# Performance work log

Measured on AMD Instinct MI355X. Metric: run time of the kernel, lower is better.

## Reference

```python
import jax, jax.numpy as jnp
import numpy as np

N = 50000          # nodes
E = 800000         # edges (before self-loops)
IN = 128           # in_channels
C = 32             # hidden_channels
H = 4              # heads
SLOPE = 0.2        # PyG GATConv default negative_slope
NUM_CLASSES = 2


def setup_inputs() -> dict:
    key = jax.random.key(0)
    ks = jax.random.split(key, 20)
    s = 0.1
    inp = {
        "x": jax.random.normal(ks[0], (N, IN), jnp.float32),
        "edge_index": jax.random.randint(ks[1], (2, E), 0, N, jnp.int64),
        # conv1: IN -> H*C (concat)
        "W1": jax.random.normal(ks[2], (IN, H * C), jnp.float32) * s,
        "a1_src": jax.random.normal(ks[3], (H, C), jnp.float32) * s,
        "a1_dst": jax.random.normal(ks[4], (H, C), jnp.float32) * s,
        "b1": jnp.zeros((H * C,), jnp.float32),
        # conv2: H*C -> H*C (concat)
        "W2": jax.random.normal(ks[5], (H * C, H * C), jnp.float32) * s,
        "a2_src": jax.random.normal(ks[6], (H, C), jnp.float32) * s,
        "a2_dst": jax.random.normal(ks[7], (H, C), jnp.float32) * s,
        "b2": jnp.zeros((H * C,), jnp.float32),
        # conv3: H*C -> C (heads=1, concat=False)
        "W3": jax.random.normal(ks[8], (H * C, C), jnp.float32) * s,
        "a3_src": jax.random.normal(ks[9], (1, C), jnp.float32) * s,
        "a3_dst": jax.random.normal(ks[10], (1, C), jnp.float32) * s,
        "b3": jnp.zeros((C,), jnp.float32),
        # node classification head: C -> 2
        "Wc": jax.random.normal(ks[11], (C, NUM_CLASSES), jnp.float32) * s,
        "bc": jnp.zeros((NUM_CLASSES,), jnp.float32),
    }
    return inp


def gat_conv(x, src, dst, W, a_src, a_dst, b, heads, out_c, concat):
    """PyG-style GATConv with self-loops already appended to (src, dst)."""
    n = x.shape[0]
    h = (x @ W).reshape(n, heads, out_c)            # [N,H,C]
    al_src = jnp.sum(h * a_src, axis=-1)            # [N,H]
    al_dst = jnp.sum(h * a_dst, axis=-1)            # [N,H]
    e = al_src[src] + al_dst[dst]                   # [Et,H]
    e = jax.nn.leaky_relu(e, SLOPE)
    # numerically-stable segment softmax over edges sharing a destination
    emax = jax.ops.segment_max(e, dst, num_segments=n)   # every node has a self-loop
    e = jnp.exp(e - emax[dst])
    denom = jax.ops.segment_sum(e, dst, num_segments=n)
    alpha = e / (denom[dst] + 1e-16)                # [Et,H]
    msg = h[src] * alpha[:, :, None]                # [Et,H,C]
    out = jax.ops.segment_sum(msg, dst, num_segments=n)  # [N,H,C]
    out = out.reshape(n, heads * out_c) if concat else jnp.mean(out, axis=1)
    return out + b


def reference(x, edge_index, W1, a1_src, a1_dst, b1, W2, a2_src, a2_dst, b2,
              W3, a3_src, a3_dst, b3, Wc, bc):
    n = x.shape[0]
    loop = jnp.arange(n, dtype=edge_index.dtype)
    src = jnp.concatenate([edge_index[0], loop])
    dst = jnp.concatenate([edge_index[1], loop])
    h = jax.nn.elu(gat_conv(x, src, dst, W1, a1_src, a1_dst, b1, H, C, True))
    h = jax.nn.elu(gat_conv(h, src, dst, W2, a2_src, a2_dst, b2, H, C, True))
    h = gat_conv(h, src, dst, W3, a3_src, a3_dst, b3, 1, C, False)
    node_output = h @ Wc + bc                       # [N,2]
    link_embedding = h                              # [N,C]
    return (node_output, link_embedding)
```

## Files before the change

### kernel.cpp

```cpp
#include <hip/hip_runtime.h>
#include <math.h>

#define SLOPE 0.2f

__device__ __forceinline__ float lrelu(float x) { return x > 0.f ? x : SLOPE * x; }

__device__ __forceinline__ float bflo(unsigned int u) { return __uint_as_float(u << 16); }
__device__ __forceinline__ float bfhi(unsigned int u) { return __uint_as_float(u & 0xffff0000u); }
__device__ __forceinline__ unsigned short f2bf(float f) {
    unsigned int u = __float_as_uint(f);
    unsigned int r = u + 0x7fffu + ((u >> 16) & 1u);
    return (unsigned short)(r >> 16);
}

typedef short frag8 __attribute__((ext_vector_type(8)));
typedef float f32x4 __attribute__((ext_vector_type(4)));

__global__ __launch_bounds__(256) void wtrans_kernel(
    const float* __restrict__ W1, const float* __restrict__ W2,
    unsigned short* __restrict__ Wt1, unsigned short* __restrict__ Wt2,
    int* __restrict__ bcnt, int nbcnt)
{
    int idx = blockIdx.x * 256 + threadIdx.x;
    if (idx < nbcnt) bcnt[idx] = 0;
    const float* W = W1;
    unsigned short* Wt = Wt1;
    int i = idx;
    if (idx >= 16384) { W = W2; Wt = Wt2; i = idx - 16384; }
    int n = i >> 7, k = i & 127;
    Wt[i] = f2bf(W[k * 128 + n]);
}

#define TF_MB 64
#define TF_LDK 136

template <bool BF16IN>
__device__ __forceinline__ void transform_body(
    int bid, const void* __restrict__ xin, const unsigned short* __restrict__ Wt,
    const float* __restrict__ a_src, const float* __restrict__ a_dst,
    unsigned short* __restrict__ hout, float* __restrict__ alsrc,
    float* __restrict__ aldst, int N,
    unsigned short* xs, unsigned short* wt)
{
    constexpr int MB = TF_MB;
    constexpr int LDK = TF_LDK;

    const int node0 = bid * MB;
    const int t = threadIdx.x;

    if constexpr (BF16IN) {
        const unsigned short* xb = (const unsigned short*)xin;
        for (int i = t; i < MB * 16; i += 256) {
            int row = i >> 4, c16 = i & 15;
            uint4 v = make_uint4(0u, 0u, 0u, 0u);
            if (node0 + row < N)
                v = ((const uint4*)(xb + (size_t)(node0 + row) * 128))[c16];
            *(uint4*)&xs[row * LDK + c16 * 8] = v;
        }
    } else {
        const float* xf = (const float*)xin;
        for (int i = t; i < MB * 32; i += 256) {
            int row = i >> 5, col4 = i & 31;
            ushort4 o;
            if (node0 + row < N) {
                float4 v = ((const float4*)(xf + (size_t)(node0 + row) * 128))[col4];
                o.x = f2bf(v.x); o.y = f2bf(v.y); o.z = f2bf(v.z); o.w = f2bf(v.w);
            } else {
                o.x = o.y = o.z = o.w = 0;
            }
            *(ushort4*)&xs[row * LDK + col4 * 4] = o;
        }
    }
    for (int i = t; i < 2048; i += 256) {
        int n = i >> 4, k16 = i & 15;
        uint4 v = ((const uint4*)Wt)[i];
        *(uint4*)&wt[n * LDK + k16 * 8] = v;
    }
    __syncthreads();

    const int w    = t >> 6;
    const int lane = t & 63;
    const int r    = lane & 15;
    const int q    = lane >> 4;

    f32x4 acc[4][2];
#pragma unroll
    for (int mt = 0; mt < 4; ++mt)
#pragma unroll
        for (int nl = 0; nl < 2; ++nl)
            acc[mt][nl] = (f32x4){0.f, 0.f, 0.f, 0.f};

#pragma unroll
    for (int kk = 0; kk < 4; ++kk) {
        const int kof = kk * 32 + q * 8;
        frag8 b0 = *(const frag8*)&wt[(w * 32 + r) * LDK + kof];
        frag8 b1 = *(const frag8*)&wt[(w * 32 + 16 + r) * LDK + kof];
#pragma unroll
        for (int mt = 0; mt < 4; ++mt) {
            frag8 a = *(const frag8*)&xs[(mt * 16 + r) * LDK + kof];
            acc[mt][0] = __builtin_amdgcn_mfma_f32_16x16x32_bf16(a, b0, acc[mt][0], 0, 0, 0);
            acc[mt][1] = __builtin_amdgcn_mfma_f32_16x16x32_bf16(a, b1, acc[mt][1], 0, 0, 0);
        }
    }

    const float as0 = a_src[w * 32 + r],      ad0 = a_dst[w * 32 + r];
    const float as1 = a_src[w * 32 + 16 + r], ad1 = a_dst[w * 32 + 16 + r];
#pragma unroll
    for (int mt = 0; mt < 4; ++mt) {
#pragma unroll
        for (int reg = 0; reg < 4; ++reg) {
            float s = acc[mt][0][reg] * as0 + acc[mt][1][reg] * as1;
            float d = acc[mt][0][reg] * ad0 + acc[mt][1][reg] * ad1;
#pragma unroll
            for (int off = 1; off < 16; off <<= 1) {
                s += __shfl_xor(s, off);
                d += __shfl_xor(d, off);
            }
            if (r == 0) {
                int m = mt * 16 + q * 4 + reg;
                int n = node0 + m;
                if (n < N) {
                    alsrc[n * 4 + w] = s;
                    aldst[n * 4 + w] = d;
                }
            }
        }
    }

    __syncthreads();
#pragma unroll
    for (int mt = 0; mt < 4; ++mt)
#pragma unroll
        for (int nl = 0; nl < 2; ++nl)
#pragma unroll
            for (int reg = 0; reg < 4; ++reg) {
                int m = mt * 16 + q * 4 + reg;
                int n = w * 32 + nl * 16 + r;
                xs[m * LDK + n] = f2bf(acc[mt][nl][reg]);
            }
    __syncthreads();
    {
        int row = t >> 2, cbase = (t & 3) * 32;
        if (node0 + row < N) {
            uint4* dst = (uint4*)(hout + (size_t)(node0 + row) * 128 + cbase);
#pragma unroll
            for (int j = 0; j < 4; ++j)
                dst[j] = *(const uint4*)&xs[row * LDK + cbase + j * 8];
        }
    }
}

template <bool BF16IN>
__global__ __launch_bounds__(256) void transform_mfma_kernel(
    const void* __restrict__ xin, const unsigned short* __restrict__ Wt,
    const float* __restrict__ a_src, const float* __restrict__ a_dst,
    unsigned short* __restrict__ hout, float* __restrict__ alsrc,
    float* __restrict__ aldst, int N)
{
    __shared__ __align__(16) unsigned short xs[TF_MB * TF_LDK];
    __shared__ __align__(16) unsigned short wt[128 * TF_LDK];
    transform_body<BF16IN>(blockIdx.x, xin, Wt, a_src, a_dst, hout,
                           alsrc, aldst, N, xs, wt);
}

template <int COUT, int Hh, int NPT>
__global__ __launch_bounds__(256) void transform_kernel(
    const unsigned short* __restrict__ xin, const float* __restrict__ W,
    const float* __restrict__ a_src, const float* __restrict__ a_dst,
    unsigned short* __restrict__ hout, float* __restrict__ alsrc,
    float* __restrict__ aldst, int N)
{
    constexpr int JT = COUT / 4;
    constexpr int GROUPS = 256 / JT;
    constexpr int NB = GROUPS * NPT;
    constexpr int PAD = 4;
    __shared__ __align__(16) float xs[NB][128 + PAD];

    const int node0 = blockIdx.x * NB;
    for (int i = threadIdx.x; i < NB * 16; i += 256) {
        int row = i >> 4, c16 = i & 15;
        uint4 v = make_uint4(0u, 0u, 0u, 0u);
        if (node0 + row < N)
            v = ((const uint4*)(xin + (size_t)(node0 + row) * 128))[c16];
        float* xp = &xs[row][c16 * 8];
        xp[0] = bflo(v.x); xp[1] = bfhi(v.x);
        xp[2] = bflo(v.y); xp[3] = bfhi(v.y);
        xp[4] = bflo(v.z); xp[5] = bfhi(v.z);
        xp[6] = bflo(v.w); xp[7] = bfhi(v.w);
    }
    __syncthreads();

    const int jt = threadIdx.x % JT;
    const int g  = threadIdx.x / JT;
    const int j4 = jt * 4;

    float4 acc[NPT];
#pragma unroll
    for (int m = 0; m < NPT; ++m) acc[m] = make_float4(0.f, 0.f, 0.f, 0.f);

    const float4* Wf4 = (const float4*)W;
    for (int k4 = 0; k4 < 32; ++k4) {
        float4 w0 = Wf4[(4 * k4 + 0) * JT + jt];
        float4 w1 = Wf4[(4 * k4 + 1) * JT + jt];
        float4 w2 = Wf4[(4 * k4 + 2) * JT + jt];
        float4 w3 = Wf4[(4 * k4 + 3) * JT + jt];
#pragma unroll
        for (int m = 0; m < NPT; ++m) {
            float4 xv = *(const float4*)&xs[g * NPT + m][k4 << 2];
            acc[m].x += xv.x * w0.x + xv.y * w1.x + xv.z * w2.x + xv.w * w3.x;
            acc[m].y += xv.x * w0.y + xv.y * w1.y + xv.z * w2.y + xv.w * w3.y;
            acc[m].z += xv.x * w0.z + xv.y * w1.z + xv.z * w2.z + xv.w * w3.z;
            acc[m].w += xv.x * w0.w + xv.y * w1.w + xv.z * w2.w + xv.w * w3.w;
        }
    }

    const float4 as4 = ((const float4*)a_src)[jt];
    const float4 ad4 = ((const float4*)a_dst)[jt];
    const int hh = j4 >> 5;

#pragma unroll
    for (int m = 0; m < NPT; ++m) {
        int n = node0 + g * NPT + m;
        float4 v = acc[m];
        float sv = v.x * as4.x + v.y * as4.y + v.z * as4.z + v.w * as4.w;
        float dv = v.x * ad4.x + v.y * ad4.y + v.z * ad4.z + v.w * ad4.w;
#pragma unroll
        for (int off = 4; off >= 1; off >>= 1) {
            sv += __shfl_xor(sv, off);
            dv += __shfl_xor(dv, off);
        }
        if (n < N) {
            ushort4 hp;
            hp.x = f2bf(v.x); hp.y = f2bf(v.y);
            hp.z = f2bf(v.z); hp.w = f2bf(v.w);
            ((ushort4*)(hout + (size_t)n * COUT))[jt] = hp;
            if ((jt & 7) == 0) {
                alsrc[n * Hh + hh] = sv;
                aldst[n * Hh + hh] = dv;
            }
        }
    }
}

#define BKT_CAP 2048
#define NBKT_MAX 1024
#define CH_BIN 4096

__device__ __forceinline__ void bin_body(
    int bid, const int* __restrict__ src, const int* __restrict__ dst,
    int* __restrict__ bcnt, unsigned int* __restrict__ tmp, int E, int nbkt,
    int* hist, int* base)
{
    const int e0 = bid * CH_BIN;
    const int e1 = min(e0 + CH_BIN, E);

    for (int b = threadIdx.x; b < nbkt; b += 256) hist[b] = 0;
    __syncthreads();
    for (int e = e0 + threadIdx.x; e < e1; e += 256) {
        int d = __builtin_nontemporal_load(dst + e);
        atomicAdd(&hist[d >> 6], 1);
    }
    __syncthreads();
    for (int b = threadIdx.x; b < nbkt; b += 256) {
        int c = hist[b];
        base[b] = (c > 0) ? atomicAdd(&bcnt[b << 4], c) : 0;
        hist[b] = 0;
    }
    __syncthreads();
    for (int e = e0 + threadIdx.x; e < e1; e += 256) {
        int d = __builtin_nontemporal_load(dst + e);
        int s = __builtin_nontemporal_load(src + e);
        int b = d >> 6;
        int pos = base[b] + atomicAdd(&hist[b], 1);
        if (pos < BKT_CAP)
            tmp[((size_t)b << 11) + pos] =
                ((unsigned int)s << 6) | (unsigned int)(d & 63);
    }
}

template <bool BF16IN>
__global__ __launch_bounds__(256) void bin_transform_kernel(
    const int* __restrict__ src, const int* __restrict__ dst,
    int* __restrict__ bcnt, unsigned int* __restrict__ tmp, int E, int nbkt,
    const void* __restrict__ xin, const unsigned short* __restrict__ Wt,
    const float* __restrict__ a_src, const float* __restrict__ a_dst,
    unsigned short* __restrict__ hout, float* __restrict__ alsrc,
    float* __restrict__ aldst, int N, int nbin)
{
    __shared__ __align__(16) unsigned short smem[TF_MB * TF_LDK + 128 * TF_LDK];
    if ((int)blockIdx.x < nbin) {
        int* hist = (int*)smem;
        bin_body(blockIdx.x, src, dst, bcnt, tmp, E, nbkt, hist, hist + NBKT_MAX);
    } else {
        transform_body<BF16IN>(blockIdx.x - nbin, xin, Wt, a_src, a_dst,
                               hout, alsrc, aldst, N, smem, smem + TF_MB * TF_LDK);
    }
}

__global__ __launch_bounds__(256) void bucket_csr_kernel(
    const unsigned int* __restrict__ tmp, const int* __restrict__ bcnt,
    int* __restrict__ deg, int* __restrict__ offsets,
    int* __restrict__ src_sorted, int N)
{
    int b = blockIdx.x;
    __shared__ int hist[64];
    if (threadIdx.x < 64) hist[threadIdx.x] = 0;
    __syncthreads();
    int cnt = min(bcnt[b << 4], BKT_CAP);
    const unsigned int* tb = tmp + ((size_t)b << 11);
    for (int i = threadIdx.x; i < cnt; i += 256)
        atomicAdd(&hist[tb[i] & 63u], 1);
    __syncthreads();
    if (threadIdx.x < 64) {
        int v = hist[threadIdx.x];
        int incl = v;
#pragma unroll
        for (int off = 1; off < 64; off <<= 1) {
            int t2 = __shfl_up(incl, off);
            if ((int)threadIdx.x >= off) incl += t2;
        }
        int excl = incl - v;
        int node = (b << 6) + threadIdx.x;
        if (node < N) {
            deg[node] = v;
            offsets[node] = (b << 11) + excl;
        }
        hist[threadIdx.x] = excl;
    }
    __syncthreads();
    for (int i = threadIdx.x; i < cnt; i += 256) {
        unsigned int p = tb[i];
        int pos = atomicAdd(&hist[p & 63u], 1);
        src_sorted[((size_t)b << 11) + pos] = (int)(p >> 6);
    }
}

__device__ __forceinline__ void fma8(const uint4& p, float w, float* a) {
    a[0] += w * bflo(p.x); a[1] += w * bfhi(p.x);
    a[2] += w * bflo(p.y); a[3] += w * bfhi(p.y);
    a[4] += w * bflo(p.z); a[5] += w * bfhi(p.z);
    a[6] += w * bflo(p.w); a[7] += w * bfhi(p.w);
}

template <int Hh, int Cc, bool DO_ELU, bool OUTBF, bool FUSE_HEAD>
__global__ __launch_bounds__(256) void gat_agg_kernel(
    const int* __restrict__ offsets, const int* __restrict__ deg_arr,
    const int* __restrict__ src_sorted,
    const unsigned short* __restrict__ h, const float* __restrict__ alsrc,
    const float* __restrict__ aldst, const float* __restrict__ bias,
    void* __restrict__ outv, const float* __restrict__ Wc,
    const float* __restrict__ bc, float* __restrict__ node_out, int N)
{
    constexpr int HC  = Hh * Cc;
    constexpr int TPN = HC / 8;
    constexpr int NPB = 256 / TPN;
    constexpr int CHUNK = 32;
    constexpr int CH_STRIDE = CHUNK + 4;
    constexpr int PLANE = NPB * CH_STRIDE + 8;
    __shared__ int   s_src[NPB][CHUNK];
    __shared__ __align__(16) float s_w[Hh * PLANE];
    __shared__ int   s_nch[NPB];

    const int g  = threadIdx.x / TPN;
    const int lt = threadIdx.x % TPN;
    const int n  = blockIdx.x * NPB + g;
    const bool valid = n < N;

    int off0 = 0, deg = 0;
    if (valid) { off0 = offsets[n]; deg = deg_arr[n]; }
    if (lt == 0) s_nch[g] = (deg + CHUNK - 1) / CHUNK;
    __syncthreads();
    int maxch = 0;
#pragma unroll
    for (int i = 0; i < NPB; ++i) maxch = max(maxch, s_nch[i]);

    const int hh = (lt * 8) / Cc;
    float adv[Hh];
    if (valid) {
        if constexpr (Hh == 4) {
            float4 t = ((const float4*)aldst)[n];
            adv[0] = t.x; adv[1] = t.y; adv[2] = t.z; adv[3] = t.w;
        } else {
            adv[0] = aldst[n];
        }
    }

    const uint4* h4 = (const uint4*)h;

    uint4 pself = make_uint4(0u, 0u, 0u, 0u);
    float als_self = 0.f;
    if (valid) {
        pself = h4[(size_t)n * TPN + lt];
        als_self = alsrc[n * Hh + hh];
    }

    const int wbase = hh * PLANE + g * CH_STRIDE;

    float a[8] = {0.f, 0.f, 0.f, 0.f, 0.f, 0.f, 0.f, 0.f};
    float den = 0.f;
    for (int ch = 0; ch < maxch; ++ch) {
        int base = ch * CHUNK;
        int cnt = deg - base;
        cnt = cnt < 0 ? 0 : (cnt > CHUNK ? CHUNK : cnt);
        __syncthreads();
        for (int i = lt; i < cnt; i += TPN) {
            int s = __builtin_nontemporal_load(src_sorted + off0 + base + i);
            s_src[g][i] = s;
            if constexpr (Hh == 4) {
                float4 av = ((const float4*)alsrc)[s];
                s_w[0 * PLANE + g * CH_STRIDE + i] = __expf(lrelu(av.x + adv[0]));
                s_w[1 * PLANE + g * CH_STRIDE + i] = __expf(lrelu(av.y + adv[1]));
                s_w[2 * PLANE + g * CH_STRIDE + i] = __expf(lrelu(av.z + adv[2]));
                s_w[3 * PLANE + g * CH_STRIDE + i] = __expf(lrelu(av.w + adv[3]));
            } else {
                s_w[g * CH_STRIDE + i] = __expf(lrelu(alsrc[s] + adv[0]));
            }
        }
        __syncthreads();
        int i = 0;
        for (; i + 3 < cnt; i += 4) {
            int s0 = s_src[g][i],     s1 = s_src[g][i + 1];
            int s2 = s_src[g][i + 2], s3 = s_src[g][i + 3];
            float4 wv = *(const float4*)&s_w[wbase + i];
            uint4 p0 = h4[(size_t)s0 * TPN + lt];
            uint4 p1 = h4[(size_t)s1 * TPN + lt];
            uint4 p2 = h4[(size_t)s2 * TPN + lt];
            uint4 p3 = h4[(size_t)s3 * TPN + lt];
            fma8(p0, wv.x, a);
            fma8(p1, wv.y, a);
            fma8(p2, wv.z, a);
            fma8(p3, wv.w, a);
            den += (wv.x + wv.y) + (wv.z + wv.w);
        }
        for (; i < cnt; ++i) {
            int s0 = s_src[g][i];
            float w0 = s_w[wbase + i];
            uint4 p0 = h4[(size_t)s0 * TPN + lt];
            fma8(p0, w0, a);
            den += w0;
        }
    }

    if (valid) {
        float wself = __expf(lrelu(als_self + adv[hh]));
        fma8(pself, wself, a);
        den += wself + 1e-16f;
        float inv = 1.f / den;
        float4 bv0 = ((const float4*)bias)[lt * 2];
        float4 bv1 = ((const float4*)bias)[lt * 2 + 1];
        float o[8];
        o[0] = a[0] * inv + bv0.x; o[1] = a[1] * inv + bv0.y;
        o[2] = a[2] * inv + bv0.z; o[3] = a[3] * inv + bv0.w;
        o[4] = a[4] * inv + bv1.x; o[5] = a[5] * inv + bv1.y;
        o[6] = a[6] * inv + bv1.z; o[7] = a[7] * inv + bv1.w;
        if (DO_ELU) {
#pragma unroll
            for (int q = 0; q < 8; ++q)
                o[q] = o[q] > 0.f ? o[q] : __expf(o[q]) - 1.f;
        }
        if constexpr (OUTBF) {
            unsigned short* ob = (unsigned short*)outv;
            uint4 pk;
            pk.x = (unsigned int)f2bf(o[0]) | ((unsigned int)f2bf(o[1]) << 16);
            pk.y = (unsigned int)f2bf(o[2]) | ((unsigned int)f2bf(o[3]) << 16);
            pk.z = (unsigned int)f2bf(o[4]) | ((unsigned int)f2bf(o[5]) << 16);
            pk.w = (unsigned int)f2bf(o[6]) | ((unsigned int)f2bf(o[7]) << 16);
            ((uint4*)(ob + (size_t)n * HC))[lt] = pk;
        } else {
            float* of = (float*)outv;
            float4* op = (float4*)(of + (size_t)n * HC);
            op[lt * 2]     = make_float4(o[0], o[1], o[2], o[3]);
            op[lt * 2 + 1] = make_float4(o[4], o[5], o[6], o[7]);
        }
        if constexpr (FUSE_HEAD) {
            float s0 = 0.f, s1 = 0.f;
#pragma unroll
            for (int q = 0; q < 8; ++q) {
                int c = lt * 8 + q;
                s0 += o[q] * Wc[c * 2];
                s1 += o[q] * Wc[c * 2 + 1];
            }
            s0 += __shfl_xor(s0, 1); s0 += __shfl_xor(s0, 2);
            s1 += __shfl_xor(s1, 1); s1 += __shfl_xor(s1, 2);
            if (lt == 0) {
                node_out[(size_t)n * 2]     = s0 + bc[0];
                node_out[(size_t)n * 2 + 1] = s1 + bc[1];
            }
        }
    }
}

extern "C" void kernel_launch(void* const* d_in, const int* in_sizes, int n_in,
                              void* d_out, int out_size, void* d_ws, size_t ws_size,
                              hipStream_t stream)
{
    const float* x   = (const float*)d_in[0];
    const int*   ei  = (const int*)d_in[1];
    const float* W1  = (const float*)d_in[2];
    const float* a1s = (const float*)d_in[3];
    const float* a1d = (const float*)d_in[4];
    const float* b1  = (const float*)d_in[5];
    const float* W2  = (const float*)d_in[6];
    const float* a2s = (const float*)d_in[7];
    const float* a2d = (const float*)d_in[8];
    const float* b2  = (const float*)d_in[9];
    const float* W3  = (const float*)d_in[10];
    const float* a3s = (const float*)d_in[11];
    const float* a3d = (const float*)d_in[12];
    const float* b3  = (const float*)d_in[13];
    const float* Wc  = (const float*)d_in[14];
    const float* bc  = (const float*)d_in[15];

    const int N = in_sizes[0] / 128;
    const int E = in_sizes[1] / 2;
    const int* srcIdx = ei;
    const int* dstIdx = ei + E;

    const int NBKT = (N + 63) >> 6;

    float* alsrc = (float*)d_ws;
    float* aldst = alsrc + (size_t)N * 4;
    unsigned short* fb16 = (unsigned short*)(aldst + (size_t)N * 4);
    unsigned short* hbuf = fb16 + (size_t)N * 128;
    int* deg        = (int*)(hbuf + (size_t)N * 128);
    int* offsets    = deg + N;
    uintptr_t wp = ((uintptr_t)(offsets + N) + 15) & ~(uintptr_t)15;
    unsigned short* wt1 = (unsigned short*)wp;
    unsigned short* wt2 = wt1 + 16384;
    int* bcnt       = (int*)(wt2 + 16384);
    int* src_sorted = bcnt + (size_t)NBKT * 16;
    unsigned int* tmp = (unsigned int*)(src_sorted + (size_t)NBKT * BKT_CAP);

    float* node_out = (float*)d_out;
    float* link_out = node_out + (size_t)N * 2;

    const int nbBin = (E + CH_BIN - 1) / CH_BIN;
    const int nbT   = (N + 63) / 64;

    wtrans_kernel<<<128, 256, 0, stream>>>(W1, W2, wt1, wt2, bcnt, NBKT * 16);

    bin_transform_kernel<false><<<nbBin + nbT, 256, 0, stream>>>(
        srcIdx, dstIdx, bcnt, tmp, E, NBKT,
        x, wt1, a1s, a1d, hbuf, alsrc, aldst, N, nbBin);

    bucket_csr_kernel<<<NBKT, 256, 0, stream>>>(tmp, bcnt, deg, offsets,
                                                src_sorted, N);

    gat_agg_kernel<4, 32, true, true, false><<<(N + 15) / 16, 256, 0, stream>>>(
        offsets, deg, src_sorted, hbuf, alsrc, aldst, b1, fb16,
        nullptr, nullptr, nullptr, N);

    transform_mfma_kernel<true><<<nbT, 256, 0, stream>>>(
        fb16, wt2, a2s, a2d, hbuf, alsrc, aldst, N);
    gat_agg_kernel<4, 32, true, true, false><<<(N + 15) / 16, 256, 0, stream>>>(
        offsets, deg, src_sorted, hbuf, alsrc, aldst, b2, fb16,
        nullptr, nullptr, nullptr, N);

    transform_kernel<32, 1, 4><<<(N + 127) / 128, 256, 0, stream>>>(
        fb16, W3, a3s, a3d, hbuf, alsrc, aldst, N);
    gat_agg_kernel<1, 32, false, false, true><<<(N + 63) / 64, 256, 0, stream>>>(
        offsets, deg, src_sorted, hbuf, alsrc, aldst, b3, link_out,
        Wc, bc, node_out, N);
}
```

Before: 271.3 us.

## Fuse layer aggregation with next-layer linear transform into single kernels

Merges each layer's GAT aggregation with the following layer's weight transform. The aggregated features stay in shared memory (bf16 for the MFMA layer-2 path, fp32 for the VALU layer-3 path) and never round-trip through global memory. Each layer gets its own h/alpha buffers, so the fused kernels never read and write the same buffer. This removes two launches and the intermediate feature writes and reads. In exchange, each block now handles 64 nodes in four sequential 16-node passes with more __syncthreads, and it holds the large shared-memory footprint during the aggregation phase, which may lower occupancy and hide less of the gather latency.

```diff
diff --git a/kernel.cpp b/kernel.cpp
--- a/kernel.cpp
+++ b/kernel.cpp
@@ -34,50 +34,14 @@
 #define TF_MB 64
 #define TF_LDK 136
 
-template <bool BF16IN>
-__device__ __forceinline__ void transform_body(
-    int bid, const void* __restrict__ xin, const unsigned short* __restrict__ Wt,
-    const float* __restrict__ a_src, const float* __restrict__ a_dst,
+__device__ __forceinline__ void transform_compute(
+    int node0, const float* __restrict__ a_src, const float* __restrict__ a_dst,
     unsigned short* __restrict__ hout, float* __restrict__ alsrc,
     float* __restrict__ aldst, int N,
-    unsigned short* xs, unsigned short* wt)
-{
-    constexpr int MB = TF_MB;
+    unsigned short* xs, const unsigned short* wt)
+{
     constexpr int LDK = TF_LDK;
-
-    const int node0 = bid * MB;
     const int t = threadIdx.x;
-
-    if constexpr (BF16IN) {
-        const unsigned short* xb = (const unsigned short*)xin;
-        for (int i = t; i < MB * 16; i += 256) {
-            int row = i >> 4, c16 = i & 15;
-            uint4 v = make_uint4(0u, 0u, 0u, 0u);
-            if (node0 + row < N)
-                v = ((const uint4*)(xb + (size_t)(node0 + row) * 128))[c16];
-            *(uint4*)&xs[row * LDK + c16 * 8] = v;
-        }
-    } else {
-        const float* xf = (const float*)xin;
-        for (int i = t; i < MB * 32; i += 256) {
-            int row = i >> 5, col4 = i & 31;
-            ushort4 o;
-            if (node0 + row < N) {
-                float4 v = ((const float4*)(xf + (size_t)(node0 + row) * 128))[col4];
-                o.x = f2bf(v.x); o.y = f2bf(v.y); o.z = f2bf(v.z); o.w = f2bf(v.w);
-            } else {
-                o.x = o.y = o.z = o.w = 0;
-            }
-            *(ushort4*)&xs[row * LDK + col4 * 4] = o;
-        }
-    }
-    for (int i = t; i < 2048; i += 256) {
-        int n = i >> 4, k16 = i & 15;
-        uint4 v = ((const uint4*)Wt)[i];
-        *(uint4*)&wt[n * LDK + k16 * 8] = v;
-    }
-    __syncthreads();
-
     const int w    = t >> 6;
     const int lane = t & 63;
     const int r    = lane & 15;
@@ -150,96 +114,35 @@
     }
 }
 
-template <bool BF16IN>
-__global__ __launch_bounds__(256) void transform_mfma_kernel(
-    const void* __restrict__ xin, const unsigned short* __restrict__ Wt,
+__device__ __forceinline__ void transform_body_f32(
+    int bid, const float* __restrict__ xf, const unsigned short* __restrict__ Wt,
     const float* __restrict__ a_src, const float* __restrict__ a_dst,
     unsigned short* __restrict__ hout, float* __restrict__ alsrc,
-    float* __restrict__ aldst, int N)
-{
-    __shared__ __align__(16) unsigned short xs[TF_MB * TF_LDK];
-    __shared__ __align__(16) unsigned short wt[128 * TF_LDK];
-    transform_body<BF16IN>(blockIdx.x, xin, Wt, a_src, a_dst, hout,
-                           alsrc, aldst, N, xs, wt);
-}
-
-template <int COUT, int Hh, int NPT>
-__global__ __launch_bounds__(256) void transform_kernel(
-    const unsigned short* __restrict__ xin, const float* __restrict__ W,
-    const float* __restrict__ a_src, const float* __restrict__ a_dst,
-    unsigned short* __restrict__ hout, float* __restrict__ alsrc,
-    float* __restrict__ aldst, int N)
-{
-    constexpr int JT = COUT / 4;
-    constexpr int GROUPS = 256 / JT;
-    constexpr int NB = GROUPS * NPT;
-    constexpr int PAD = 4;
-    __shared__ __align__(16) float xs[NB][128 + PAD];
-
-    const int node0 = blockIdx.x * NB;
-    for (int i = threadIdx.x; i < NB * 16; i += 256) {
-        int row = i >> 4, c16 = i & 15;
-        uint4 v = make_uint4(0u, 0u, 0u, 0u);
-        if (node0 + row < N)
-            v = ((const uint4*)(xin + (size_t)(node0 + row) * 128))[c16];
-        float* xp = &xs[row][c16 * 8];
-        xp[0] = bflo(v.x); xp[1] = bfhi(v.x);
-        xp[2] = bflo(v.y); xp[3] = bfhi(v.y);
-        xp[4] = bflo(v.z); xp[5] = bfhi(v.z);
-        xp[6] = bflo(v.w); xp[7] = bfhi(v.w);
-    }
-    __syncthreads();
-
-    const int jt = threadIdx.x % JT;
-    const int g  = threadIdx.x / JT;
-    const int j4 = jt * 4;
-
-    float4 acc[NPT];
-#pragma unroll
-    for (int m = 0; m < NPT; ++m) acc[m] = make_float4(0.f, 0.f, 0.f, 0.f);
-
-    const float4* Wf4 = (const float4*)W;
-    for (int k4 = 0; k4 < 32; ++k4) {
-        float4 w0 = Wf4[(4 * k4 + 0) * JT + jt];
-        float4 w1 = Wf4[(4 * k4 + 1) * JT + jt];
-        float4 w2 = Wf4[(4 * k4 + 2) * JT + jt];
-        float4 w3 = Wf4[(4 * k4 + 3) * JT + jt];
-#pragma unroll
-        for (int m = 0; m < NPT; ++m) {
-            float4 xv = *(const float4*)&xs[g * NPT + m][k4 << 2];
-            acc[m].x += xv.x * w0.x + xv.y * w1.x + xv.z * w2.x + xv.w * w3.x;
-            acc[m].y += xv.x * w0.y + xv.y * w1.y + xv.z * w2.y + xv.w * w3.y;
-            acc[m].z += xv.x * w0.z + xv.y * w1.z + xv.z * w2.z + xv.w * w3.z;
-            acc[m].w += xv.x * w0.w + xv.y * w1.w + xv.z * w2.w + xv.w * w3.w;
-        }
-    }
-
-    const float4 as4 = ((const float4*)a_src)[jt];
-    const float4 ad4 = ((const float4*)a_dst)[jt];
-    const int hh = j4 >> 5;
-
-#pragma unroll
-    for (int m = 0; m < NPT; ++m) {
-        int n = node0 + g * NPT + m;
-        float4 v = acc[m];
-        float sv = v.x * as4.x + v.y * as4.y + v.z * as4.z + v.w * as4.w;
-        float dv = v.x * ad4.x + v.y * ad4.y + v.z * ad4.z + v.w * ad4.w;
-#pragma unroll
-        for (int off = 4; off >= 1; off >>= 1) {
-            sv += __shfl_xor(sv, off);
-            dv += __shfl_xor(dv, off);
-        }
-        if (n < N) {
-            ushort4 hp;
-            hp.x = f2bf(v.x); hp.y = f2bf(v.y);
-            hp.z = f2bf(v.z); hp.w = f2bf(v.w);
-            ((ushort4*)(hout + (size_t)n * COUT))[jt] = hp;
-            if ((jt & 7) == 0) {
-                alsrc[n * Hh + hh] = sv;
-                aldst[n * Hh + hh] = dv;
-            }
-        }
-    }
+    float* __restrict__ aldst, int N,
+    unsigned short* xs, unsigned short* wt)
+{
+    constexpr int LDK = TF_LDK;
+    const int node0 = bid * TF_MB;
+    const int t = threadIdx.x;
+
+    for (int i = t; i < TF_MB * 32; i += 256) {
+        int row = i >> 5, col4 = i & 31;
+        ushort4 o;
+        if (node0 + row < N) {
+            float4 v = ((const float4*)(xf + (size_t)(node0 + row) * 128))[col4];
+            o.x = f2bf(v.x); o.y = f2bf(v.y); o.z = f2bf(v.z); o.w = f2bf(v.w);
+        } else {
+            o.x = o.y = o.z = o.w = 0;
+        }
+        *(ushort4*)&xs[row * LDK + col4 * 4] = o;
+    }
+    for (int i = t; i < 2048; i += 256) {
+        int n = i >> 4, k16 = i & 15;
+        uint4 v = ((const uint4*)Wt)[i];
+        *(uint4*)&wt[n * LDK + k16 * 8] = v;
+    }
+    __syncthreads();
+    transform_compute(node0, a_src, a_dst, hout, alsrc, aldst, N, xs, wt);
 }
 
 #define BKT_CAP 2048
@@ -278,11 +181,10 @@
     }
 }
 
-template <bool BF16IN>
 __global__ __launch_bounds__(256) void bin_transform_kernel(
     const int* __restrict__ src, const int* __restrict__ dst,
     int* __restrict__ bcnt, unsigned int* __restrict__ tmp, int E, int nbkt,
-    const void* __restrict__ xin, const unsigned short* __restrict__ Wt,
+    const float* __restrict__ xin, const unsigned short* __restrict__ Wt,
     const float* __restrict__ a_src, const float* __restrict__ a_dst,
     unsigned short* __restrict__ hout, float* __restrict__ alsrc,
     float* __restrict__ aldst, int N, int nbin)
@@ -292,8 +194,8 @@
         int* hist = (int*)smem;
         bin_body(blockIdx.x, src, dst, bcnt, tmp, E, nbkt, hist, hist + NBKT_MAX);
     } else {
-        transform_body<BF16IN>(blockIdx.x - nbin, xin, Wt, a_src, a_dst,
-                               hout, alsrc, aldst, N, smem, smem + TF_MB * TF_LDK);
+        transform_body_f32(blockIdx.x - nbin, xin, Wt, a_src, a_dst,
+                           hout, alsrc, aldst, N, smem, smem + TF_MB * TF_LDK);
     }
 }
 
@@ -335,6 +237,11 @@
     }
 }
 
+#define AG_CHUNK 32
+#define AG_STRIDE (AG_CHUNK + 4)
+#define AG_PLANE  (16 * AG_STRIDE + 8)
+#define AG_SCRATCH_INTS (16 * AG_CHUNK + 4 * AG_PLANE + 16)
+
 __device__ __forceinline__ void fma8(const uint4& p, float w, float* a) {
     a[0] += w * bflo(p.x); a[1] += w * bfhi(p.x);
     a[2] += w * bflo(p.y); a[3] += w * bfhi(p.y);
@@ -342,23 +249,237 @@
     a[6] += w * bflo(p.w); a[7] += w * bfhi(p.w);
 }
 
-template <int Hh, int Cc, bool DO_ELU, bool OUTBF, bool FUSE_HEAD>
-__global__ __launch_bounds__(256) void gat_agg_kernel(
+template <bool DO_ELU>
+__device__ __forceinline__ void agg16_node(
+    int n, bool valid, int g, int lt,
+    const int* __restrict__ offsets, const int* __restrict__ deg_arr,
+    const int* __restrict__ src_sorted, const uint4* __restrict__ h4,
+    const float* __restrict__ alsrc, const float* __restrict__ aldst,
+    const float* __restrict__ bias, int* scratch, float* o)
+{
+    int*   s_src = scratch;
+    float* s_w   = (float*)(scratch + 16 * AG_CHUNK);
+    int*   s_nch = scratch + 16 * AG_CHUNK + 4 * AG_PLANE;
+
+    int off0 = 0, deg = 0;
+    if (valid) { off0 = offsets[n]; deg = deg_arr[n]; }
+    if (lt == 0) s_nch[g] = (deg + AG_CHUNK - 1) / AG_CHUNK;
+    __syncthreads();
+    int maxch = 0;
+#pragma unroll
+    for (int i = 0; i < 16; ++i) maxch = max(maxch, s_nch[i]);
+
+    const int hh = lt >> 2;
+    float adv[4] = {0.f, 0.f, 0.f, 0.f};
+    if (valid) {
+        float4 t4 = ((const float4*)aldst)[n];
+        adv[0] = t4.x; adv[1] = t4.y; adv[2] = t4.z; adv[3] = t4.w;
+    }
+
+    uint4 pself = make_uint4(0u, 0u, 0u, 0u);
+    float als_self = 0.f;
+    if (valid) {
+        pself = h4[(size_t)n * 16 + lt];
+        als_self = alsrc[n * 4 + hh];
+    }
+
+    const int wbase = hh * AG_PLANE + g * AG_STRIDE;
+
+    float a[8] = {0.f, 0.f, 0.f, 0.f, 0.f, 0.f, 0.f, 0.f};
+    float den = 0.f;
+    for (int ch = 0; ch < maxch; ++ch) {
+        int base = ch * AG_CHUNK;
+        int cnt = deg - base;
+        cnt = cnt < 0 ? 0 : (cnt > AG_CHUNK ? AG_CHUNK : cnt);
+        __syncthreads();
+        for (int i = lt; i < cnt; i += 16) {
+            int s = __builtin_nontemporal_load(src_sorted + off0 + base + i);
+            s_src[g * AG_CHUNK + i] = s;
+            float4 av = ((const float4*)alsrc)[s];
+            s_w[0 * AG_PLANE + g * AG_STRIDE + i] = __expf(lrelu(av.x + adv[0]));
+            s_w[1 * AG_PLANE + g * AG_STRIDE + i] = __expf(lrelu(av.y + adv[1]));
+            s_w[2 * AG_PLANE + g * AG_STRIDE + i] = __expf(lrelu(av.z + adv[2]));
+            s_w[3 * AG_PLANE + g * AG_STRIDE + i] = __expf(lrelu(av.w + adv[3]));
+        }
+        __syncthreads();
+        int i = 0;
+        for (; i + 3 < cnt; i += 4) {
+            int s0 = s_src[g * AG_CHUNK + i],     s1 = s_src[g * AG_CHUNK + i + 1];
+            int s2 = s_src[g * AG_CHUNK + i + 2], s3 = s_src[g * AG_CHUNK + i + 3];
+            float4 wv = *(const float4*)&s_w[wbase + i];
+            uint4 p0 = h4[(size_t)s0 * 16 + lt];
+            uint4 p1 = h4[(size_t)s1 * 16 + lt];
+            uint4 p2 = h4[(size_t)s2 * 16 + lt];
+            uint4 p3 = h4[(size_t)s3 * 16 + lt];
+            fma8(p0, wv.x, a);
+            fma8(p1, wv.y, a);
+            fma8(p2, wv.z, a);
+            fma8(p3, wv.w, a);
+            den += (wv.x + wv.y) + (wv.z + wv.w);
+        }
+        for (; i < cnt; ++i) {
+            int s0 = s_src[g * AG_CHUNK + i];
+            float w0 = s_w[wbase + i];
+            uint4 p0 = h4[(size_t)s0 * 16 + lt];
+            fma8(p0, w0, a);
+            den += w0;
+        }
+    }
+
+    float wself = __expf(lrelu(als_self + adv[hh]));
+    fma8(pself, wself, a);
+    den += wself + 1e-16f;
+    float inv = 1.f / den;
+    float4 bv0 = ((const float4*)bias)[lt * 2];
+    float4 bv1 = ((const float4*)bias)[lt * 2 + 1];
+    o[0] = a[0] * inv + bv0.x; o[1] = a[1] * inv + bv0.y;
+    o[2] = a[2] * inv + bv0.z; o[3] = a[3] * inv + bv0.w;
+    o[4] = a[4] * inv + bv1.x; o[5] = a[5] * inv + bv1.y;
+    o[6] = a[6] * inv + bv1.z; o[7] = a[7] * inv + bv1.w;
+    if (DO_ELU) {
+#pragma unroll
+        for (int q = 0; q < 8; ++q)
+            o[q] = o[q] > 0.f ? o[q] : __expf(o[q]) - 1.f;
+    }
+}
+
+__global__ __launch_bounds__(256) void aggtrans_mfma_kernel(
     const int* __restrict__ offsets, const int* __restrict__ deg_arr,
     const int* __restrict__ src_sorted,
     const unsigned short* __restrict__ h, const float* __restrict__ alsrc,
     const float* __restrict__ aldst, const float* __restrict__ bias,
-    void* __restrict__ outv, const float* __restrict__ Wc,
+    const unsigned short* __restrict__ Wt,
+    const float* __restrict__ a_src, const float* __restrict__ a_dst,
+    unsigned short* __restrict__ hout, float* __restrict__ alsrc_o,
+    float* __restrict__ aldst_o, int N)
+{
+    __shared__ __align__(16) unsigned short xs[TF_MB * TF_LDK];
+    __shared__ __align__(16) unsigned short wt[128 * TF_LDK];
+    int* scratch = (int*)wt;
+
+    const int node0 = blockIdx.x * 64;
+    const int g  = threadIdx.x >> 4;
+    const int lt = threadIdx.x & 15;
+    const uint4* h4 = (const uint4*)h;
+
+    for (int b = 0; b < 4; ++b) {
+        int row = b * 16 + g;
+        int n = node0 + row;
+        float o[8];
+        agg16_node<true>(n, n < N, g, lt, offsets, deg_arr, src_sorted,
+                         h4, alsrc, aldst, bias, scratch, o);
+        uint4 pk;
+        pk.x = (unsigned int)f2bf(o[0]) | ((unsigned int)f2bf(o[1]) << 16);
+        pk.y = (unsigned int)f2bf(o[2]) | ((unsigned int)f2bf(o[3]) << 16);
+        pk.z = (unsigned int)f2bf(o[4]) | ((unsigned int)f2bf(o[5]) << 16);
+        pk.w = (unsigned int)f2bf(o[6]) | ((unsigned int)f2bf(o[7]) << 16);
+        *(uint4*)&xs[row * TF_LDK + lt * 8] = pk;
+    }
+    __syncthreads();
+    for (int i = threadIdx.x; i < 2048; i += 256) {
+        int nn = i >> 4, k16 = i & 15;
+        uint4 v = ((const uint4*)Wt)[i];
+        *(uint4*)&wt[nn * TF_LDK + k16 * 8] = v;
+    }
+    __syncthreads();
+    transform_compute(node0, a_src, a_dst, hout, alsrc_o, aldst_o, N, xs, wt);
+}
+
+__global__ __launch_bounds__(256) void aggtrans_valu_kernel(
+    const int* __restrict__ offsets, const int* __restrict__ deg_arr,
+    const int* __restrict__ src_sorted,
+    const unsigned short* __restrict__ h, const float* __restrict__ alsrc,
+    const float* __restrict__ aldst, const float* __restrict__ bias,
+    const float* __restrict__ W,
+    const float* __restrict__ a_src, const float* __restrict__ a_dst,
+    unsigned short* __restrict__ hout, float* __restrict__ alsrc_o,
+    float* __restrict__ aldst_o, int N)
+{
+    constexpr int LDKF = 132;
+    __shared__ __align__(16) float xs[64 * LDKF];
+    __shared__ int scratch[AG_SCRATCH_INTS];
+
+    const int node0 = blockIdx.x * 64;
+    const int g  = threadIdx.x >> 4;
+    const int lt = threadIdx.x & 15;
+    const uint4* h4 = (const uint4*)h;
+
+    for (int b = 0; b < 4; ++b) {
+        int row = b * 16 + g;
+        int n = node0 + row;
+        float o[8];
+        agg16_node<true>(n, n < N, g, lt, offsets, deg_arr, src_sorted,
+                         h4, alsrc, aldst, bias, scratch, o);
+        float* xp = &xs[row * LDKF + lt * 8];
+        ((float4*)xp)[0] = make_float4(o[0], o[1], o[2], o[3]);
+        ((float4*)xp)[1] = make_float4(o[4], o[5], o[6], o[7]);
+    }
+    __syncthreads();
+
+    const int jt = threadIdx.x & 7;
+    const int g2 = threadIdx.x >> 3;
+
+    float4 acc[2];
+    acc[0] = make_float4(0.f, 0.f, 0.f, 0.f);
+    acc[1] = make_float4(0.f, 0.f, 0.f, 0.f);
+
+    const float4* Wf4 = (const float4*)W;
+    for (int k4 = 0; k4 < 32; ++k4) {
+        float4 w0 = Wf4[(4 * k4 + 0) * 8 + jt];
+        float4 w1 = Wf4[(4 * k4 + 1) * 8 + jt];
+        float4 w2 = Wf4[(4 * k4 + 2) * 8 + jt];
+        float4 w3 = Wf4[(4 * k4 + 3) * 8 + jt];
+#pragma unroll
+        for (int m = 0; m < 2; ++m) {
+            float4 xv = *(const float4*)&xs[(g2 * 2 + m) * LDKF + (k4 << 2)];
+            acc[m].x += xv.x * w0.x + xv.y * w1.x + xv.z * w2.x + xv.w * w3.x;
+            acc[m].y += xv.x * w0.y + xv.y * w1.y + xv.z * w2.y + xv.w * w3.y;
+            acc[m].z += xv.x * w0.z + xv.y * w1.z + xv.z * w2.z + xv.w * w3.z;
+            acc[m].w += xv.x * w0.w + xv.y * w1.w + xv.z * w2.w + xv.w * w3.w;
+        }
+    }
+
+    const float4 as4 = ((const float4*)a_src)[jt];
+    const float4 ad4 = ((const float4*)a_dst)[jt];
+
+#pragma unroll
+    for (int m = 0; m < 2; ++m) {
+        int n = node0 + g2 * 2 + m;
+        float4 v = acc[m];
+        float sv = v.x * as4.x + v.y * as4.y + v.z * as4.z + v.w * as4.w;
+        float dv = v.x * ad4.x + v.y * ad4.y + v.z * ad4.z + v.w * ad4.w;
+#pragma unroll
+        for (int off = 4; off >= 1; off >>= 1) {
+            sv += __shfl_xor(sv, off);
+            dv += __shfl_xor(dv, off);
+        }
+        if (n < N) {
+            ushort4 hp;
+            hp.x = f2bf(v.x); hp.y = f2bf(v.y);
+            hp.z = f2bf(v.z); hp.w = f2bf(v.w);
+            ((ushort4*)(hout + (size_t)n * 32))[jt] = hp;
+            if (jt == 0) {
+                alsrc_o[n] = sv;
+                aldst_o[n] = dv;
+            }
+        }
+    }
+}
+
+__global__ __launch_bounds__(256) void gat_agg3_kernel(
+    const int* __restrict__ offsets, const int* __restrict__ deg_arr,
+    const int* __restrict__ src_sorted,
+    const unsigned short* __restrict__ h, const float* __restrict__ alsrc,
+    const float* __restrict__ aldst, const float* __restrict__ bias,
+    float* __restrict__ link_out, const float* __restrict__ Wc,
     const float* __restrict__ bc, float* __restrict__ node_out, int N)
 {
-    constexpr int HC  = Hh * Cc;
-    constexpr int TPN = HC / 8;
-    constexpr int NPB = 256 / TPN;
+    constexpr int TPN = 4;
+    constexpr int NPB = 64;
     constexpr int CHUNK = 32;
     constexpr int CH_STRIDE = CHUNK + 4;
-    constexpr int PLANE = NPB * CH_STRIDE + 8;
     __shared__ int   s_src[NPB][CHUNK];
-    __shared__ __align__(16) float s_w[Hh * PLANE];
+    __shared__ float s_w[NPB * CH_STRIDE + 8];
     __shared__ int   s_nch[NPB];
 
     const int g  = threadIdx.x / TPN;
@@ -371,30 +492,23 @@
     if (lt == 0) s_nch[g] = (deg + CHUNK - 1) / CHUNK;
     __syncthreads();
     int maxch = 0;
-#pragma unroll
-    for (int i = 0; i < NPB; ++i) maxch = max(maxch, s_nch[i]);
-
-    const int hh = (lt * 8) / Cc;
-    float adv[Hh];
-    if (valid) {
-        if constexpr (Hh == 4) {
-            float4 t = ((const float4*)aldst)[n];
-            adv[0] = t.x; adv[1] = t.y; adv[2] = t.z; adv[3] = t.w;
-        } else {
-            adv[0] = aldst[n];
-        }
-    }
+    for (int i = threadIdx.x & 63; i < NPB; i += 64)
+        maxch = max(maxch, s_nch[i]);
+#pragma unroll
+    for (int off = 32; off >= 1; off >>= 1)
+        maxch = max(maxch, __shfl_xor(maxch, off));
+
+    float adv0 = valid ? aldst[n] : 0.f;
 
     const uint4* h4 = (const uint4*)h;
-
     uint4 pself = make_uint4(0u, 0u, 0u, 0u);
     float als_self = 0.f;
     if (valid) {
         pself = h4[(size_t)n * TPN + lt];
-        als_self = alsrc[n * Hh + hh];
-    }
-
-    const int wbase = hh * PLANE + g * CH_STRIDE;
+        als_self = alsrc[n];
+    }
+
+    const int wbase = g * CH_STRIDE;
 
     float a[8] = {0.f, 0.f, 0.f, 0.f, 0.f, 0.f, 0.f, 0.f};
     float den = 0.f;
@@ -406,15 +520,7 @@
         for (int i = lt; i < cnt; i += TPN) {
             int s = __builtin_nontemporal_load(src_sorted + off0 + base + i);
             s_src[g][i] = s;
-            if constexpr (Hh == 4) {
-                float4 av = ((const float4*)alsrc)[s];
-                s_w[0 * PLANE + g * CH_STRIDE + i] = __expf(lrelu(av.x + adv[0]));
-                s_w[1 * PLANE + g * CH_STRIDE + i] = __expf(lrelu(av.y + adv[1]));
-                s_w[2 * PLANE + g * CH_STRIDE + i] = __expf(lrelu(av.z + adv[2]));
-                s_w[3 * PLANE + g * CH_STRIDE + i] = __expf(lrelu(av.w + adv[3]));
-            } else {
-                s_w[g * CH_STRIDE + i] = __expf(lrelu(alsrc[s] + adv[0]));
-            }
+            s_w[wbase + i] = __expf(lrelu(alsrc[s] + adv0));
         }
         __syncthreads();
         int i = 0;
@@ -442,7 +548,7 @@
     }
 
     if (valid) {
-        float wself = __expf(lrelu(als_self + adv[hh]));
+        float wself = __expf(lrelu(als_self + adv0));
         fma8(pself, wself, a);
         den += wself + 1e-16f;
         float inv = 1.f / den;
@@ -453,39 +559,21 @@
         o[2] = a[2] * inv + bv0.z; o[3] = a[3] * inv + bv0.w;
         o[4] = a[4] * inv + bv1.x; o[5] = a[5] * inv + bv1.y;
         o[6] = a[6] * inv + bv1.z; o[7] = a[7] * inv + bv1.w;
-        if (DO_ELU) {
-#pragma unroll
-            for (int q = 0; q < 8; ++q)
-                o[q] = o[q] > 0.f ? o[q] : __expf(o[q]) - 1.f;
-        }
-        if constexpr (OUTBF) {
-            unsigned short* ob = (unsigned short*)outv;
-            uint4 pk;
-            pk.x = (unsigned int)f2bf(o[0]) | ((unsigned int)f2bf(o[1]) << 16);
-            pk.y = (unsigned int)f2bf(o[2]) | ((unsigned int)f2bf(o[3]) << 16);
-            pk.z = (unsigned int)f2bf(o[4]) | ((unsigned int)f2bf(o[5]) << 16);
-            pk.w = (unsigned int)f2bf(o[6]) | ((unsigned int)f2bf(o[7]) << 16);
-            ((uint4*)(ob + (size_t)n * HC))[lt] = pk;
-        } else {
-            float* of = (float*)outv;
-            float4* op = (float4*)(of + (size_t)n * HC);
-            op[lt * 2]     = make_float4(o[0], o[1], o[2], o[3]);
-            op[lt * 2 + 1] = make_float4(o[4], o[5], o[6], o[7]);
-        }
-        if constexpr (FUSE_HEAD) {
-            float s0 = 0.f, s1 = 0.f;
-#pragma unroll
-            for (int q = 0; q < 8; ++q) {
-                int c = lt * 8 + q;
-                s0 += o[q] * Wc[c * 2];
-                s1 += o[q] * Wc[c * 2 + 1];
-            }
-            s0 += __shfl_xor(s0, 1); s0 += __shfl_xor(s0, 2);
-            s1 += __shfl_xor(s1, 1); s1 += __shfl_xor(s1, 2);
-            if (lt == 0) {
-                node_out[(size_t)n * 2]     = s0 + bc[0];
-                node_out[(size_t)n * 2 + 1] = s1 + bc[1];
-            }
+        float4* op = (float4*)(link_out + (size_t)n * 32);
+        op[lt * 2]     = make_float4(o[0], o[1], o[2], o[3]);
+        op[lt * 2 + 1] = make_float4(o[4], o[5], o[6], o[7]);
+        float s0 = 0.f, s1 = 0.f;
+#pragma unroll
+        for (int q = 0; q < 8; ++q) {
+            int c = lt * 8 + q;
+            s0 += o[q] * Wc[c * 2];
+            s1 += o[q] * Wc[c * 2 + 1];
+        }
+        s0 += __shfl_xor(s0, 1); s0 += __shfl_xor(s0, 2);
+        s1 += __shfl_xor(s1, 1); s1 += __shfl_xor(s1, 2);
+        if (lt == 0) {
+            node_out[(size_t)n * 2]     = s0 + bc[0];
+            node_out[(size_t)n * 2 + 1] = s1 + bc[1];
         }
     }
 }
@@ -518,11 +606,16 @@
 
     const int NBKT = (N + 63) >> 6;
 
-    float* alsrc = (float*)d_ws;
-    float* aldst = alsrc + (size_t)N * 4;
-    unsigned short* fb16 = (unsigned short*)(aldst + (size_t)N * 4);
-    unsigned short* hbuf = fb16 + (size_t)N * 128;
-    int* deg        = (int*)(hbuf + (size_t)N * 128);
+    float* alsrc1 = (float*)d_ws;
+    float* aldst1 = alsrc1 + (size_t)N * 4;
+    float* alsrc2 = aldst1 + (size_t)N * 4;
+    float* aldst2 = alsrc2 + (size_t)N * 4;
+    float* alsrc3 = aldst2 + (size_t)N * 4;
+    float* aldst3 = alsrc3 + (size_t)N;
+    unsigned short* h1 = (unsigned short*)(aldst3 + (size_t)N);
+    unsigned short* h2 = h1 + (size_t)N * 128;
+    unsigned short* h3 = h2 + (size_t)N * 128;
+    int* deg        = (int*)(h3 + (size_t)N * 32);
     int* offsets    = deg + N;
     uintptr_t wp = ((uintptr_t)(offsets + N) + 15) & ~(uintptr_t)15;
     unsigned short* wt1 = (unsigned short*)wp;
@@ -539,26 +632,22 @@
 
     wtrans_kernel<<<128, 256, 0, stream>>>(W1, W2, wt1, wt2, bcnt, NBKT * 16);
 
-    bin_transform_kernel<false><<<nbBin + nbT, 256, 0, stream>>>(
+    bin_transform_kernel<<<nbBin + nbT, 256, 0, stream>>>(
         srcIdx, dstIdx, bcnt, tmp, E, NBKT,
-        x, wt1, a1s, a1d, hbuf, alsrc, aldst, N, nbBin);
+        x, wt1, a1s, a1d, h1, alsrc1, aldst1, N, nbBin);
 
     bucket_csr_kernel<<<NBKT, 256, 0, stream>>>(tmp, bcnt, deg, offsets,
                                                 src_sorted, N);
 
-    gat_agg_kernel<4, 32, true, true, false><<<(N + 15) / 16, 256, 0, stream>>>(
-        offsets, deg, src_sorted, hbuf, alsrc, aldst, b1, fb16,
-        nullptr, nullptr, nullptr, N);
-
-    transform_mfma_kernel<true><<<nbT, 256, 0, stream>>>(
-        fb16, wt2, a2s, a2d, hbuf, alsrc, aldst, N);
-    gat_agg_kernel<4, 32, true, true, false><<<(N + 15) / 16, 256, 0, stream>>>(
-        offsets, deg, src_sorted, hbuf, alsrc, aldst, b2, fb16,
-        nullptr, nullptr, nullptr, N);
-
-    transform_kernel<32, 1, 4><<<(N + 127) / 128, 256, 0, stream>>>(
-        fb16, W3, a3s, a3d, hbuf, alsrc, aldst, N);
-    gat_agg_kernel<1, 32, false, false, true><<<(N + 63) / 64, 256, 0, stream>>>(
-        offsets, deg, src_sorted, hbuf, alsrc, aldst, b3, link_out,
+    aggtrans_mfma_kernel<<<nbT, 256, 0, stream>>>(
+        offsets, deg, src_sorted, h1, alsrc1, aldst1, b1,
+        wt2, a2s, a2d, h2, alsrc2, aldst2, N);
+
+    aggtrans_valu_kernel<<<nbT, 256, 0, stream>>>(
+        offsets, deg, src_sorted, h2, alsrc2, aldst2, b2,
+        W3, a3s, a3d, h3, alsrc3, aldst3, N);
+
+    gat_agg3_kernel<<<nbT, 256, 0, stream>>>(
+        offsets, deg, src_sorted, h3, alsrc3, aldst3, b3, link_out,
         Wc, bc, node_out, N);
 }
```

Result: slower. 428.8 us (+58.1%).

## Drop shared-memory edge staging in GAT aggregation; compute weights per thread directly

Applied to the files above, without the earlier changes.

The aggregation kernel no longer stages source indices and softmax weights in shared memory chunk by chunk with block-wide barriers. Each thread now reads the edge list and alsrc directly and computes its own head's exp weight, so invalid nodes can return early. Launch bounds also ask for higher occupancy. This removes the barriers and the lockstep wait on the block's highest-degree node, at the cost of redundant index loads and exp evaluations across the threads that share a node.

```diff
diff --git a/kernel.cpp b/kernel.cpp
--- a/kernel.cpp
+++ b/kernel.cpp
@@ -278,11 +278,10 @@
     }
 }
 
-template <bool BF16IN>
 __global__ __launch_bounds__(256) void bin_transform_kernel(
     const int* __restrict__ src, const int* __restrict__ dst,
     int* __restrict__ bcnt, unsigned int* __restrict__ tmp, int E, int nbkt,
-    const void* __restrict__ xin, const unsigned short* __restrict__ Wt,
+    const float* __restrict__ xin, const unsigned short* __restrict__ Wt,
     const float* __restrict__ a_src, const float* __restrict__ a_dst,
     unsigned short* __restrict__ hout, float* __restrict__ alsrc,
     float* __restrict__ aldst, int N, int nbin)
@@ -292,8 +291,8 @@
         int* hist = (int*)smem;
         bin_body(blockIdx.x, src, dst, bcnt, tmp, E, nbkt, hist, hist + NBKT_MAX);
     } else {
-        transform_body<BF16IN>(blockIdx.x - nbin, xin, Wt, a_src, a_dst,
-                               hout, alsrc, aldst, N, smem, smem + TF_MB * TF_LDK);
+        transform_body<false>(blockIdx.x - nbin, xin, Wt, a_src, a_dst,
+                              hout, alsrc, aldst, N, smem, smem + TF_MB * TF_LDK);
     }
 }
 
@@ -343,7 +342,7 @@
 }
 
 template <int Hh, int Cc, bool DO_ELU, bool OUTBF, bool FUSE_HEAD>
-__global__ __launch_bounds__(256) void gat_agg_kernel(
+__global__ __launch_bounds__(256, 8) void gat_agg_kernel(
     const int* __restrict__ offsets, const int* __restrict__ deg_arr,
     const int* __restrict__ src_sorted,
     const unsigned short* __restrict__ h, const float* __restrict__ alsrc,
@@ -354,97 +353,59 @@
     constexpr int HC  = Hh * Cc;
     constexpr int TPN = HC / 8;
     constexpr int NPB = 256 / TPN;
-    constexpr int CHUNK = 32;
-    constexpr int CH_STRIDE = CHUNK + 4;
-    constexpr int PLANE = NPB * CH_STRIDE + 8;
-    __shared__ int   s_src[NPB][CHUNK];
-    __shared__ __align__(16) float s_w[Hh * PLANE];
-    __shared__ int   s_nch[NPB];
 
     const int g  = threadIdx.x / TPN;
     const int lt = threadIdx.x % TPN;
     const int n  = blockIdx.x * NPB + g;
-    const bool valid = n < N;
-
-    int off0 = 0, deg = 0;
-    if (valid) { off0 = offsets[n]; deg = deg_arr[n]; }
-    if (lt == 0) s_nch[g] = (deg + CHUNK - 1) / CHUNK;
-    __syncthreads();
-    int maxch = 0;
-#pragma unroll
-    for (int i = 0; i < NPB; ++i) maxch = max(maxch, s_nch[i]);
-
-    const int hh = (lt * 8) / Cc;
-    float adv[Hh];
-    if (valid) {
-        if constexpr (Hh == 4) {
-            float4 t = ((const float4*)aldst)[n];
-            adv[0] = t.x; adv[1] = t.y; adv[2] = t.z; adv[3] = t.w;
-        } else {
-            adv[0] = aldst[n];
-        }
-    }
-
+    if (n >= N) return;
+
+    const int off0 = offsets[n];
+    const int deg  = deg_arr[n];
+    const int hh   = (lt * 8) / Cc;
+    const float adv = aldst[(size_t)n * Hh + hh];
     const uint4* h4 = (const uint4*)h;
-
-    uint4 pself = make_uint4(0u, 0u, 0u, 0u);
-    float als_self = 0.f;
-    if (valid) {
-        pself = h4[(size_t)n * TPN + lt];
-        als_self = alsrc[n * Hh + hh];
-    }
-
-    const int wbase = hh * PLANE + g * CH_STRIDE;
+    const int* el = src_sorted + off0;
 
     float a[8] = {0.f, 0.f, 0.f, 0.f, 0.f, 0.f, 0.f, 0.f};
-    float den = 0.f;
-    for (int ch = 0; ch < maxch; ++ch) {
-        int base = ch * CHUNK;
-        int cnt = deg - base;
-        cnt = cnt < 0 ? 0 : (cnt > CHUNK ? CHUNK : cnt);
-        __syncthreads();
-        for (int i = lt; i < cnt; i += TPN) {
-            int s = __builtin_nontemporal_load(src_sorted + off0 + base + i);
-            s_src[g][i] = s;
-            if constexpr (Hh == 4) {
-                float4 av = ((const float4*)alsrc)[s];
-                s_w[0 * PLANE + g * CH_STRIDE + i] = __expf(lrelu(av.x + adv[0]));
-                s_w[1 * PLANE + g * CH_STRIDE + i] = __expf(lrelu(av.y + adv[1]));
-                s_w[2 * PLANE + g * CH_STRIDE + i] = __expf(lrelu(av.z + adv[2]));
-                s_w[3 * PLANE + g * CH_STRIDE + i] = __expf(lrelu(av.w + adv[3]));
-            } else {
-                s_w[g * CH_STRIDE + i] = __expf(lrelu(alsrc[s] + adv[0]));
-            }
-        }
-        __syncthreads();
-        int i = 0;
-        for (; i + 3 < cnt; i += 4) {
-            int s0 = s_src[g][i],     s1 = s_src[g][i + 1];
-            int s2 = s_src[g][i + 2], s3 = s_src[g][i + 3];
-            float4 wv = *(const float4*)&s_w[wbase + i];
-            uint4 p0 = h4[(size_t)s0 * TPN + lt];
-            uint4 p1 = h4[(size_t)s1 * TPN + lt];
-            uint4 p2 = h4[(size_t)s2 * TPN + lt];
-            uint4 p3 = h4[(size_t)s3 * TPN + lt];
-            fma8(p0, wv.x, a);
-            fma8(p1, wv.y, a);
-            fma8(p2, wv.z, a);
-            fma8(p3, wv.w, a);
-            den += (wv.x + wv.y) + (wv.z + wv.w);
-        }
-        for (; i < cnt; ++i) {
-            int s0 = s_src[g][i];
-            float w0 = s_w[wbase + i];
-            uint4 p0 = h4[(size_t)s0 * TPN + lt];
-            fma8(p0, w0, a);
-            den += w0;
-        }
-    }
-
-    if (valid) {
-        float wself = __expf(lrelu(als_self + adv[hh]));
-        fma8(pself, wself, a);
-        den += wself + 1e-16f;
+
+    float den;
+    {
+        float wself = __expf(lrelu(alsrc[(size_t)n * Hh + hh] + adv));
+        fma8(h4[(size_t)n * TPN + lt], wself, a);
+        den = wself + 1e-16f;
+    }
+
+    int e = 0;
+    for (; e + 3 < deg; e += 4) {
+        int s0 = el[e], s1 = el[e + 1], s2 = el[e + 2], s3 = el[e + 3];
+        float l0 = alsrc[(size_t)s0 * Hh + hh];
+        float l1 = alsrc[(size_t)s1 * Hh + hh];
+        float l2 = alsrc[(size_t)s2 * Hh + hh];
+        float l3 = alsrc[(size_t)s3 * Hh + hh];
+        uint4 p0 = h4[(size_t)s0 * TPN + lt];
+        uint4 p1 = h4[(size_t)s1 * TPN + lt];
+        uint4 p2 = h4[(size_t)s2 * TPN + lt];
+        uint4 p3 = h4[(size_t)s3 * TPN + lt];
+        float w0 = __expf(lrelu(l0 + adv));
+        float w1 = __expf(lrelu(l1 + adv));
+        float w2 = __expf(lrelu(l2 + adv));
+        float w3 = __expf(lrelu(l3 + adv));
+        fma8(p0, w0, a);
+        fma8(p1, w1, a);
+        fma8(p2, w2, a);
+        fma8(p3, w3, a);
+        den += (w0 + w1) + (w2 + w3);
+    }
+    for (; e < deg; ++e) {
+        int s0 = el[e];
+        float l0 = alsrc[(size_t)s0 * Hh + hh];
+        uint4 p0 = h4[(size_t)s0 * TPN + lt];
+        float w0 = __expf(lrelu(l0 + adv));
+        fma8(p0, w0, a);
+        den += w0;
+    }
+
+    {
         float inv = 1.f / den;
         float4 bv0 = ((const float4*)bias)[lt * 2];
         float4 bv1 = ((const float4*)bias)[lt * 2 + 1];
@@ -539,7 +500,7 @@
 
     wtrans_kernel<<<128, 256, 0, stream>>>(W1, W2, wt1, wt2, bcnt, NBKT * 16);
 
-    bin_transform_kernel<false><<<nbBin + nbT, 256, 0, stream>>>(
+    bin_transform_kernel<<<nbBin + nbT, 256, 0, stream>>>(
         srcIdx, dstIdx, bcnt, tmp, E, NBKT,
         x, wt1, a1s, a1d, hbuf, alsrc, aldst, N, nbBin);
 
```

Result: no change. 271.1 us (-0.1%).
